# Kernel optimization log

Measured on AMD Instinct MI355X. Metric: run time of the kernel, lower is better.

The kernel has to match this reference:

```python
import jax, jax.numpy as jnp
import numpy as np

N = 50000       # nodes
E = 800000      # edges (before self-loops)
F_IN = 256      # input feature dim
HID = 32        # hidden per head
HEADS = 4
CLASSES = 32


def setup_inputs() -> dict:
    key = jax.random.key(0)
    ks = jax.random.split(key, 10)
    x = jax.random.normal(ks[0], (N, F_IN), dtype=jnp.float32)
    edge_index = jax.random.randint(ks[1], (2, E), 0, N, dtype=jnp.int32)
    s1 = 1.0 / np.sqrt(F_IN)
    s2 = 1.0 / np.sqrt(HEADS * HID)
    W1 = jax.random.normal(ks[2], (HEADS * HID, F_IN), dtype=jnp.float32) * s1
    a_src1 = jax.random.normal(ks[3], (HEADS, HID), dtype=jnp.float32) * 0.1
    a_dst1 = jax.random.normal(ks[4], (HEADS, HID), dtype=jnp.float32) * 0.1
    b1 = jnp.zeros((HEADS * HID,), dtype=jnp.float32)
    W2 = jax.random.normal(ks[5], (CLASSES, HEADS * HID), dtype=jnp.float32) * s2
    a_src2 = jax.random.normal(ks[6], (1, CLASSES), dtype=jnp.float32) * 0.1
    a_dst2 = jax.random.normal(ks[7], (1, CLASSES), dtype=jnp.float32) * 0.1
    b2 = jnp.zeros((CLASSES,), dtype=jnp.float32)
    return {"x": x, "edge_index": edge_index,
            "W1": W1, "a_src1": a_src1, "a_dst1": a_dst1, "b1": b1,
            "W2": W2, "a_src2": a_src2, "a_dst2": a_dst2, "b2": b2}


def gat_conv(x, src, dst, W, a_src, a_dst, b, heads, ch):
    """PyG GATConv: linear -> per-head additive attention -> segment softmax over dst -> scatter-sum."""
    n = x.shape[0]
    h = (x @ W.T).reshape(n, heads, ch)                      # [N,H,C]
    asc = jnp.einsum('nhc,hc->nh', h, a_src)                 # att_src . h_j
    adc = jnp.einsum('nhc,hc->nh', h, a_dst)                 # att_dst . h_i
    e = jax.nn.leaky_relu(asc[src] + adc[dst], 0.2)          # [E,H]
    m = jax.ops.segment_max(e, dst, num_segments=n)          # stable softmax per destination
    p = jnp.exp(e - m[dst])
    denom = jax.ops.segment_sum(p, dst, num_segments=n)
    alpha = p / (denom[dst] + 1e-16)                         # [E,H]
    out = jax.ops.segment_sum(h[src] * alpha[:, :, None], dst, num_segments=n)  # [N,H,C]
    return out.reshape(n, heads * ch) + b


def reference(x, edge_index, W1, a_src1, a_dst1, b1, W2, a_src2, a_dst2, b2):
    # PyG GATConv default add_self_loops=True
    loops = jnp.arange(N, dtype=edge_index.dtype)
    src = jnp.concatenate([edge_index[0], loops])
    dst = jnp.concatenate([edge_index[1], loops])
    h = gat_conv(x, src, dst, W1, a_src1, a_dst1, b1, HEADS, HID)
    h = jax.nn.relu(h)                                       # dropout is identity in eval mode
    out = gat_conv(h, src, dst, W2, a_src2, a_dst2, b2, 1, CLASSES)
    return jax.nn.log_softmax(out, axis=1)
```

## Files before the change

kernel.cpp:

```cpp
#include <hip/hip_runtime.h>
#include <hip/hip_fp16.h>

#define N_NODES 50000
#define E_EDGES 800000
#define ET (E_EDGES + N_NODES)
#define NBKT 1024
#define BCAP 2048
#define G1_BLOCKS 391
#define P_BLOCKS 250
#define P_EPB 3200

typedef _Float16 h8 __attribute__((ext_vector_type(8)));
typedef float f32x16 __attribute__((ext_vector_type(16)));

__device__ __forceinline__ float lrelu(float v) { return v > 0.f ? v : 0.2f * v; }

__global__ __launch_bounds__(256) void prep_kernel(const float* __restrict__ W1,
                                                   const float* __restrict__ W2,
                                                   const float* __restrict__ as1,
                                                   const float* __restrict__ ad1,
                                                   _Float16* __restrict__ w1h,
                                                   _Float16* __restrict__ w2h,
                                                   int* __restrict__ cursor) {
    int i = blockIdx.x * 256 + threadIdx.x;
    if (i < 1024) cursor[i] = 0;
    if (i < 4096) {
        int j = i * 8;
#pragma unroll
        for (int t = 0; t < 8; t++) w1h[j + t] = (_Float16)W1[j + t];
    } else if (i < 4608) {
        int j = (i - 4096) * 8;
#pragma unroll
        for (int t = 0; t < 8; t++) w2h[j + t] = (_Float16)W2[j + t];
    } else if (i < 5376) {
        int j = (i - 4608) * 8;
#pragma unroll
        for (int t = 0; t < 8; t++) w1h[136 * 256 + j + t] = (_Float16)0.f;
    } else if (i < 7424) {
        int a = i - 5376;
        int h = a >> 8, k = a & 255;
        const float* av = (h < 4 ? as1 : ad1) + (h & 3) * 32;
        const float* wb = W1 + (size_t)(h & 3) * 32 * 256 + k;
        float s = 0.f;
#pragma unroll
        for (int c = 0; c < 32; c++) s += av[c] * wb[(size_t)c * 256];
        w1h[(size_t)(128 + h) * 256 + k] = (_Float16)s;
    }
}

__global__ __launch_bounds__(256) void gp_kernel(const float* __restrict__ x,
                                                 const int* __restrict__ ei,
                                                 const _Float16* __restrict__ w1h,
                                                 _Float16* __restrict__ h1h,
                                                 float* __restrict__ asc1,
                                                 float* __restrict__ adc1,
                                                 int* __restrict__ cursor,
                                                 int* __restrict__ scratch) {
    __shared__ int hcnt[NBKT];
    __shared__ int hbase[NBKT];
    int tid = threadIdx.x;
    if (blockIdx.x >= G1_BLOCKS) {
        int b = blockIdx.x - G1_BLOCKS;
#pragma unroll
        for (int u = 0; u < NBKT / 256; u++) hcnt[u * 256 + tid] = 0;
        __syncthreads();
        int e0 = b * P_EPB;
        const int4* s4 = (const int4*)(ei + e0);
        const int4* d4 = (const int4*)(ei + E_EDGES + e0);
        for (int q = tid; q < P_EPB / 4; q += 256) {
            int4 d = d4[q];
            atomicAdd(&hcnt[d.x >> 6], 1);
            atomicAdd(&hcnt[d.y >> 6], 1);
            atomicAdd(&hcnt[d.z >> 6], 1);
            atomicAdd(&hcnt[d.w >> 6], 1);
        }
        __syncthreads();
#pragma unroll
        for (int u = 0; u < NBKT / 256; u++) {
            int bb = u * 256 + tid;
            int c = hcnt[bb];
            hbase[bb] = (c > 0) ? atomicAdd(&cursor[bb], c) : 0;
            hcnt[bb] = 0;
        }
        __syncthreads();
        for (int q = tid; q < P_EPB / 4; q += 256) {
            int4 s = s4[q];
            int4 d = d4[q];
            int bk, pos;
            bk = d.x >> 6; pos = hbase[bk] + atomicAdd(&hcnt[bk], 1);
            scratch[(size_t)bk * BCAP + pos] = s.x | ((d.x & 63) << 16);
            bk = d.y >> 6; pos = hbase[bk] + atomicAdd(&hcnt[bk], 1);
            scratch[(size_t)bk * BCAP + pos] = s.y | ((d.y & 63) << 16);
            bk = d.z >> 6; pos = hbase[bk] + atomicAdd(&hcnt[bk], 1);
            scratch[(size_t)bk * BCAP + pos] = s.z | ((d.z & 63) << 16);
            bk = d.w >> 6; pos = hbase[bk] + atomicAdd(&hcnt[bk], 1);
            scratch[(size_t)bk * BCAP + pos] = s.w | ((d.w & 63) << 16);
        }
        return;
    }
    int wid = tid >> 6, lane = tid & 63;
    int rbase = blockIdx.x * 128 + wid * 32;
    if (rbase >= N_NODES) return;
    int l31 = lane & 31, l5 = lane >> 5;
    int ar = rbase + l31;
    if (ar > N_NODES - 1) ar = N_NODES - 1;
    const float* ap = x + (size_t)ar * 256 + l5 * 8;
    const _Float16* bp = w1h + (size_t)l31 * 256 + l5 * 8;
    f32x16 acc0 = {}, acc1 = {}, acc2 = {}, acc3 = {}, acc4 = {};
#pragma unroll 4
    for (int ks = 0; ks < 16; ks++) {
        float4 xa = *(const float4*)(ap + ks * 16);
        float4 xb = *(const float4*)(ap + ks * 16 + 4);
        h8 av;
        av[0] = (_Float16)xa.x; av[1] = (_Float16)xa.y;
        av[2] = (_Float16)xa.z; av[3] = (_Float16)xa.w;
        av[4] = (_Float16)xb.x; av[5] = (_Float16)xb.y;
        av[6] = (_Float16)xb.z; av[7] = (_Float16)xb.w;
        h8 b0 = *(const h8*)(bp + ks * 16);
        h8 b1 = *(const h8*)(bp + 32 * 256 + ks * 16);
        h8 b2 = *(const h8*)(bp + 64 * 256 + ks * 16);
        h8 b3 = *(const h8*)(bp + 96 * 256 + ks * 16);
        h8 b4 = *(const h8*)(bp + 128 * 256 + ks * 16);
        acc0 = __builtin_amdgcn_mfma_f32_32x32x16_f16(av, b0, acc0, 0, 0, 0);
        acc1 = __builtin_amdgcn_mfma_f32_32x32x16_f16(av, b1, acc1, 0, 0, 0);
        acc2 = __builtin_amdgcn_mfma_f32_32x32x16_f16(av, b2, acc2, 0, 0, 0);
        acc3 = __builtin_amdgcn_mfma_f32_32x32x16_f16(av, b3, acc3, 0, 0, 0);
        acc4 = __builtin_amdgcn_mfma_f32_32x32x16_f16(av, b4, acc4, 0, 0, 0);
    }
#pragma unroll
    for (int j = 0; j < 16; j++) {
        int row = rbase + (j & 3) + 8 * (j >> 2) + 4 * l5;
        if (row < N_NODES) {
            h1h[(size_t)row * 128 + 0  + l31] = (_Float16)acc0[j];
            h1h[(size_t)row * 128 + 32 + l31] = (_Float16)acc1[j];
            h1h[(size_t)row * 128 + 64 + l31] = (_Float16)acc2[j];
            h1h[(size_t)row * 128 + 96 + l31] = (_Float16)acc3[j];
            float v4 = acc4[j];
            if (l31 < 4) asc1[(size_t)row * 4 + l31] = v4;
            else if (l31 < 8) adc1[(size_t)row * 4 + (l31 - 4)] = v4;
        }
    }
}

__global__ __launch_bounds__(256) void fine_kernel(const int* __restrict__ scratch,
                                                   const int* __restrict__ cursor,
                                                   const float* __restrict__ asc1,
                                                   const float* __restrict__ adc1,
                                                   int* __restrict__ off,
                                                   int4* __restrict__ combo,
                                                   int* __restrict__ srcs) {
    __shared__ int rec[BCAP];
    __shared__ int fh[64];
    __shared__ int fcur[64];
    __shared__ int red[256];
    int b = blockIdx.x;
    int tid = threadIdx.x;
    int cnt = cursor[b];
    int part = 0;
    for (int i = tid; i < b; i += 256) part += cursor[i];
    red[tid] = part;
    if (tid < 64) fh[tid] = (b * 64 + tid < N_NODES) ? 1 : 0;
    __syncthreads();
    for (int s = 128; s >= 1; s >>= 1) {
        if (tid < s) red[tid] += red[tid + s];
        __syncthreads();
    }
    int gbase = red[0] + b * 64;
    for (int k = tid; k < cnt; k += 256) {
        int r = scratch[(size_t)b * BCAP + k];
        rec[k] = r;
        atomicAdd(&fh[r >> 16], 1);
    }
    __syncthreads();
    if (tid < 64) {
        int v = fh[tid];
        int incl = v;
#pragma unroll
        for (int d = 1; d < 64; d <<= 1) {
            int u = __shfl_up(incl, d);
            if (tid >= d) incl += u;
        }
        int excl = incl - v;
        fcur[tid] = excl;
        int n = b * 64 + tid;
        if (n < N_NODES) off[n] = gbase + excl;
    }
    if (b == 781 && tid == 0) off[N_NODES] = ET;
    __syncthreads();
    if (tid < 64) {
        int n = b * 64 + tid;
        if (n < N_NODES) {
            int pos = gbase + atomicAdd(&fcur[tid], 1);
            float4 av = *(const float4*)(asc1 + (size_t)n * 4);
            float4 dv = *(const float4*)(adc1 + (size_t)n * 4);
            __half2 p01 = __floats2half2_rn(__expf(lrelu(av.x + dv.x)), __expf(lrelu(av.y + dv.y)));
            __half2 p23 = __floats2half2_rn(__expf(lrelu(av.z + dv.z)), __expf(lrelu(av.w + dv.w)));
            int4 o;
            o.x = n;
            o.y = *(int*)&p01;
            o.z = *(int*)&p23;
            o.w = 0;
            combo[pos] = o;
            srcs[pos] = n;
        }
    }
    for (int k = tid; k < cnt; k += 256) {
        int r = rec[k];
        int src = r & 0xFFFF;
        int fbin = r >> 16;
        int dst = b * 64 + fbin;
        int pos = gbase + atomicAdd(&fcur[fbin], 1);
        float4 av = *(const float4*)(asc1 + (size_t)src * 4);
        float4 dv = *(const float4*)(adc1 + (size_t)dst * 4);
        __half2 p01 = __floats2half2_rn(__expf(lrelu(av.x + dv.x)), __expf(lrelu(av.y + dv.y)));
        __half2 p23 = __floats2half2_rn(__expf(lrelu(av.z + dv.z)), __expf(lrelu(av.w + dv.w)));
        int4 o;
        o.x = src;
        o.y = *(int*)&p01;
        o.z = *(int*)&p23;
        o.w = 0;
        combo[pos] = o;
        srcs[pos] = src;
    }
}

__global__ __launch_bounds__(256) void agg1_kernel(const __half* __restrict__ h1h,
                                                   const int4* __restrict__ combo,
                                                   const float* __restrict__ b1,
                                                   const int* __restrict__ off,
                                                   __half* __restrict__ h1b) {
    int wid = threadIdx.x >> 6, lane = threadIdx.x & 63;
    int node = blockIdx.x * 4 + wid;
    if (node >= N_NODES) return;
    int hh = lane >> 4;
    const __half2* h1h2 = (const __half2*)h1h;
    int s0 = off[node], s1 = off[node + 1];
    float den = 0.f, a0 = 0.f, a1 = 0.f;
    int j = s0;
    for (; j + 8 <= s1; j += 8) {
        int4 c[8];
#pragma unroll
        for (int u = 0; u < 8; u++) c[u] = combo[j + u];
        __half2 hv[8];
#pragma unroll
        for (int u = 0; u < 8; u++) hv[u] = h1h2[(size_t)c[u].x * 64 + lane];
#pragma unroll
        for (int u = 0; u < 8; u++) {
            union { int u32; __half2 h; } v;
            v.u32 = (hh & 2) ? c[u].z : c[u].y;
            float p = __half2float((hh & 1) ? v.h.y : v.h.x);
            float2 f = __half22float2(hv[u]);
            den += p;
            a0 += p * f.x;
            a1 += p * f.y;
        }
    }
    for (; j + 4 <= s1; j += 4) {
        int4 c[4];
#pragma unroll
        for (int u = 0; u < 4; u++) c[u] = combo[j + u];
        __half2 hv[4];
#pragma unroll
        for (int u = 0; u < 4; u++) hv[u] = h1h2[(size_t)c[u].x * 64 + lane];
#pragma unroll
        for (int u = 0; u < 4; u++) {
            union { int u32; __half2 h; } v;
            v.u32 = (hh & 2) ? c[u].z : c[u].y;
            float p = __half2float((hh & 1) ? v.h.y : v.h.x);
            float2 f = __half22float2(hv[u]);
            den += p;
            a0 += p * f.x;
            a1 += p * f.y;
        }
    }
    for (; j < s1; j++) {
        int4 c = combo[j];
        union { int u32; __half2 h; } v;
        v.u32 = (hh & 2) ? c.z : c.y;
        float p = __half2float((hh & 1) ? v.h.y : v.h.x);
        float2 f = __half22float2(h1h2[(size_t)c.x * 64 + lane]);
        den += p;
        a0 += p * f.x;
        a1 += p * f.y;
    }
    float inv = 1.f / (den + 1e-16f);
    float o0 = fmaxf(a0 * inv + b1[2 * lane], 0.f);
    float o1 = fmaxf(a1 * inv + b1[2 * lane + 1], 0.f);
    ((__half2*)h1b)[(size_t)node * 64 + lane] = __floats2half2_rn(o0, o1);
}

__global__ __launch_bounds__(256) void gemm2_mfma(const __half* __restrict__ h1b,
                                                  const _Float16* __restrict__ w2h,
                                                  const float* __restrict__ as2,
                                                  const float* __restrict__ ad2,
                                                  __half* __restrict__ h2h,
                                                  float* __restrict__ asc2,
                                                  float* __restrict__ adc2) {
    int wid = threadIdx.x >> 6, lane = threadIdx.x & 63;
    int rbase = blockIdx.x * 128 + wid * 32;
    if (rbase >= N_NODES) return;
    int l31 = lane & 31, l5 = lane >> 5;
    int ar = rbase + l31;
    if (ar > N_NODES - 1) ar = N_NODES - 1;
    const _Float16* ap = (const _Float16*)h1b + (size_t)ar * 128 + l5 * 8;
    const _Float16* bp = w2h + (size_t)l31 * 128 + l5 * 8;
    f32x16 acc = {};
#pragma unroll
    for (int ks = 0; ks < 8; ks++) {
        h8 av = *(const h8*)(ap + ks * 16);
        h8 bv = *(const h8*)(bp + ks * 16);
        acc = __builtin_amdgcn_mfma_f32_32x32x16_f16(av, bv, acc, 0, 0, 0);
    }
    float asw = as2[l31], adw = ad2[l31];
#pragma unroll
    for (int j = 0; j < 16; j++) {
        int row = rbase + (j & 3) + 8 * (j >> 2) + 4 * l5;
        float v = acc[j];
        float sv = v * asw, dv = v * adw;
#pragma unroll
        for (int m = 1; m <= 16; m <<= 1) {
            sv += __shfl_xor(sv, m);
            dv += __shfl_xor(dv, m);
        }
        if (row < N_NODES) {
            h2h[(size_t)row * 32 + l31] = __float2half(v);
            if (l31 == 0) { asc2[row] = sv; adc2[row] = dv; }
        }
    }
}

__global__ __launch_bounds__(256) void agg2_kernel(const __half* __restrict__ h2h,
                                                   const int* __restrict__ srcs,
                                                   const float* __restrict__ asc2,
                                                   const float* __restrict__ adc2,
                                                   const float* __restrict__ b2,
                                                   const int* __restrict__ off,
                                                   float* __restrict__ out) {
    int wid = threadIdx.x >> 6, lane = threadIdx.x & 63;
    int node = blockIdx.x * 4 + wid;
    if (node >= N_NODES) return;
    int g = lane >> 4;
    int li = lane & 15;
    const __half2* h2h2 = (const __half2*)h2h;
    float adv = adc2[node];
    int s0 = off[node], s1 = off[node + 1];
    float den = 0.f, a0 = 0.f, a1 = 0.f;
    int j = s0 + g;
    for (; j + 16 <= s1; j += 16) {
        int s[4];
#pragma unroll
        for (int u = 0; u < 4; u++) s[u] = srcs[j + 4 * u];
        float av[4];
#pragma unroll
        for (int u = 0; u < 4; u++) av[u] = asc2[s[u]];
        __half2 hv[4];
#pragma unroll
        for (int u = 0; u < 4; u++) hv[u] = h2h2[(size_t)s[u] * 16 + li];
#pragma unroll
        for (int u = 0; u < 4; u++) {
            float p = __expf(lrelu(av[u] + adv));
            float2 f = __half22float2(hv[u]);
            den += p;
            a0 += p * f.x;
            a1 += p * f.y;
        }
    }
    for (; j < s1; j += 4) {
        int s = srcs[j];
        float p = __expf(lrelu(asc2[s] + adv));
        float2 f = __half22float2(h2h2[(size_t)s * 16 + li]);
        den += p;
        a0 += p * f.x;
        a1 += p * f.y;
    }
    den += __shfl_xor(den, 16); den += __shfl_xor(den, 32);
    a0 += __shfl_xor(a0, 16);  a0 += __shfl_xor(a0, 32);
    a1 += __shfl_xor(a1, 16);  a1 += __shfl_xor(a1, 32);
    float inv = 1.f / (den + 1e-16f);
    float v0 = a0 * inv + b2[2 * li];
    float v1 = a1 * inv + b2[2 * li + 1];
    float mx = fmaxf(v0, v1);
#pragma unroll
    for (int msk = 8; msk >= 1; msk >>= 1) mx = fmaxf(mx, __shfl_xor(mx, msk));
    float se = __expf(v0 - mx) + __expf(v1 - mx);
#pragma unroll
    for (int msk = 8; msk >= 1; msk >>= 1) se += __shfl_xor(se, msk);
    float lse = mx + __logf(se);
    if (lane < 16) {
        ((float2*)out)[(size_t)node * 16 + li] = make_float2(v0 - lse, v1 - lse);
    }
}

extern "C" void kernel_launch(void* const* d_in, const int* in_sizes, int n_in,
                              void* d_out, int out_size, void* d_ws, size_t ws_size,
                              hipStream_t stream) {
    const float* x   = (const float*)d_in[0];
    const int* ei    = (const int*)d_in[1];
    const float* W1  = (const float*)d_in[2];
    const float* as1 = (const float*)d_in[3];
    const float* ad1 = (const float*)d_in[4];
    const float* b1  = (const float*)d_in[5];
    const float* W2  = (const float*)d_in[6];
    const float* as2 = (const float*)d_in[7];
    const float* ad2 = (const float*)d_in[8];
    const float* b2  = (const float*)d_in[9];
    float* out = (float*)d_out;

    char* base = (char*)d_ws;
    int4* combo   = (int4*)base;
    int* scratch  = (int*)(base + 13600000);
    _Float16* w1h = (_Float16*)(base + 30377216);
    _Float16* w2h = (_Float16*)(base + 30459136);
    _Float16* h1h = (_Float16*)(base + 30467328);
    __half* h1b   = (__half*)(base + 43267328);
    __half* h2h   = (__half*)(base + 56067328);
    float* asc1   = (float*)(base + 59267328);
    float* adc1   = (float*)(base + 60067328);
    float* asc2   = (float*)(base + 60867328);
    float* adc2   = (float*)(base + 61067328);
    int* off      = (int*)(base + 61267328);
    int* cursor   = (int*)(base + 61467332);
    int* srcs     = (int*)(base + 61471428);

    prep_kernel<<<29, 256, 0, stream>>>(W1, W2, as1, ad1, w1h, w2h, cursor);
    gp_kernel<<<G1_BLOCKS + P_BLOCKS, 256, 0, stream>>>(x, ei, w1h, h1h, asc1, adc1, cursor, scratch);
    fine_kernel<<<782, 256, 0, stream>>>(scratch, cursor, asc1, adc1, off, combo, srcs);
    agg1_kernel<<<(N_NODES + 3) / 4, 256, 0, stream>>>((const __half*)h1h, combo, b1, off, h1b);
    gemm2_mfma<<<391, 256, 0, stream>>>(h1b, w2h, as2, ad2, h2h, asc2, adc2);
    agg2_kernel<<<(N_NODES + 3) / 4, 256, 0, stream>>>(h2h, srcs, asc2, adc2, b2, off, out);
}
```

Baseline: 138.9 us.

## Fuse fine CSR bucketing with layer-1 aggregation using shared-memory edge lists

Merges fine_kernel and agg1_kernel into a single 512-thread kernel. Each block builds its 64-destination edge list (sources and fp16 attention weights) in LDS and then aggregates those nodes directly from shared memory. This drops the global combo buffer write/read round trip and one kernel launch. In exchange, each block uses much more LDS, which can lower occupancy, and aggregation parallelism drops to 8 nodes per wave, serialised, in only 782 blocks. Degree imbalance within a bucket could also leave waves idle.

```diff
diff --git a/kernel.cpp b/kernel.cpp
--- a/kernel.cpp
+++ b/kernel.cpp
@@ -6,6 +6,7 @@
 #define ET (E_EDGES + N_NODES)
 #define NBKT 1024
 #define BCAP 2048
+#define SCAP 2112
 #define G1_BLOCKS 391
 #define P_BLOCKS 250
 #define P_EPB 3200
@@ -142,38 +143,45 @@
     }
 }
 
-__global__ __launch_bounds__(256) void fine_kernel(const int* __restrict__ scratch,
-                                                   const int* __restrict__ cursor,
-                                                   const float* __restrict__ asc1,
-                                                   const float* __restrict__ adc1,
-                                                   int* __restrict__ off,
-                                                   int4* __restrict__ combo,
-                                                   int* __restrict__ srcs) {
+__global__ __launch_bounds__(512) void fa_kernel(const int* __restrict__ scratch,
+                                                 const int* __restrict__ cursor,
+                                                 const float* __restrict__ asc1,
+                                                 const float* __restrict__ adc1,
+                                                 const __half* __restrict__ h1h,
+                                                 const float* __restrict__ b1,
+                                                 int* __restrict__ off,
+                                                 int* __restrict__ srcs,
+                                                 __half* __restrict__ h1b) {
     __shared__ int rec[BCAP];
+    __shared__ int ssrc[SCAP];
+    __shared__ int sp01[SCAP];
+    __shared__ int sp23[SCAP];
     __shared__ int fh[64];
     __shared__ int fcur[64];
-    __shared__ int red[256];
+    __shared__ int lstart[64];
+    __shared__ int red[512];
     int b = blockIdx.x;
     int tid = threadIdx.x;
     int cnt = cursor[b];
     int part = 0;
-    for (int i = tid; i < b; i += 256) part += cursor[i];
+    for (int i = tid; i < b; i += 512) part += cursor[i];
     red[tid] = part;
-    if (tid < 64) fh[tid] = (b * 64 + tid < N_NODES) ? 1 : 0;
+    if (tid < 64) fh[tid] = 0;
     __syncthreads();
-    for (int s = 128; s >= 1; s >>= 1) {
+    for (int s = 256; s >= 1; s >>= 1) {
         if (tid < s) red[tid] += red[tid + s];
         __syncthreads();
     }
     int gbase = red[0] + b * 64;
-    for (int k = tid; k < cnt; k += 256) {
+    for (int k = tid; k < cnt; k += 512) {
         int r = scratch[(size_t)b * BCAP + k];
         rec[k] = r;
         atomicAdd(&fh[r >> 16], 1);
     }
     __syncthreads();
     if (tid < 64) {
-        int v = fh[tid];
+        int n = b * 64 + tid;
+        int v = fh[tid] + ((n < N_NODES) ? 1 : 0);
         int incl = v;
 #pragma unroll
         for (int d = 1; d < 64; d <<= 1) {
@@ -181,8 +189,8 @@
             if (tid >= d) incl += u;
         }
         int excl = incl - v;
-        fcur[tid] = excl;
-        int n = b * 64 + tid;
+        lstart[tid] = excl;
+        fcur[tid] = excl + ((n < N_NODES) ? 1 : 0);
         if (n < N_NODES) off[n] = gbase + excl;
     }
     if (b == 781 && tid == 0) off[N_NODES] = ET;
@@ -190,103 +198,102 @@
     if (tid < 64) {
         int n = b * 64 + tid;
         if (n < N_NODES) {
-            int pos = gbase + atomicAdd(&fcur[tid], 1);
+            int pos = lstart[tid];
             float4 av = *(const float4*)(asc1 + (size_t)n * 4);
             float4 dv = *(const float4*)(adc1 + (size_t)n * 4);
             __half2 p01 = __floats2half2_rn(__expf(lrelu(av.x + dv.x)), __expf(lrelu(av.y + dv.y)));
             __half2 p23 = __floats2half2_rn(__expf(lrelu(av.z + dv.z)), __expf(lrelu(av.w + dv.w)));
-            int4 o;
-            o.x = n;
-            o.y = *(int*)&p01;
-            o.z = *(int*)&p23;
-            o.w = 0;
-            combo[pos] = o;
-            srcs[pos] = n;
-        }
-    }
-    for (int k = tid; k < cnt; k += 256) {
+            ssrc[pos] = n;
+            sp01[pos] = *(int*)&p01;
+            sp23[pos] = *(int*)&p23;
+            srcs[gbase + pos] = n;
+        }
+    }
+    for (int k = tid; k < cnt; k += 512) {
         int r = rec[k];
         int src = r & 0xFFFF;
         int fbin = r >> 16;
         int dst = b * 64 + fbin;
-        int pos = gbase + atomicAdd(&fcur[fbin], 1);
+        int pos = atomicAdd(&fcur[fbin], 1);
         float4 av = *(const float4*)(asc1 + (size_t)src * 4);
         float4 dv = *(const float4*)(adc1 + (size_t)dst * 4);
         __half2 p01 = __floats2half2_rn(__expf(lrelu(av.x + dv.x)), __expf(lrelu(av.y + dv.y)));
         __half2 p23 = __floats2half2_rn(__expf(lrelu(av.z + dv.z)), __expf(lrelu(av.w + dv.w)));
-        int4 o;
-        o.x = src;
-        o.y = *(int*)&p01;
-        o.z = *(int*)&p23;
-        o.w = 0;
-        combo[pos] = o;
-        srcs[pos] = src;
-    }
-}
-
-__global__ __launch_bounds__(256) void agg1_kernel(const __half* __restrict__ h1h,
-                                                   const int4* __restrict__ combo,
-                                                   const float* __restrict__ b1,
-                                                   const int* __restrict__ off,
-                                                   __half* __restrict__ h1b) {
-    int wid = threadIdx.x >> 6, lane = threadIdx.x & 63;
-    int node = blockIdx.x * 4 + wid;
-    if (node >= N_NODES) return;
+        ssrc[pos] = src;
+        sp01[pos] = *(int*)&p01;
+        sp23[pos] = *(int*)&p23;
+        srcs[gbase + pos] = src;
+    }
+    __syncthreads();
+    int wid = tid >> 6, lane = tid & 63;
     int hh = lane >> 4;
     const __half2* h1h2 = (const __half2*)h1h;
-    int s0 = off[node], s1 = off[node + 1];
-    float den = 0.f, a0 = 0.f, a1 = 0.f;
-    int j = s0;
-    for (; j + 8 <= s1; j += 8) {
-        int4 c[8];
-#pragma unroll
-        for (int u = 0; u < 8; u++) c[u] = combo[j + u];
-        __half2 hv[8];
-#pragma unroll
-        for (int u = 0; u < 8; u++) hv[u] = h1h2[(size_t)c[u].x * 64 + lane];
-#pragma unroll
-        for (int u = 0; u < 8; u++) {
+    float bl0 = b1[2 * lane], bl1 = b1[2 * lane + 1];
+    for (int ln = wid * 8; ln < wid * 8 + 8; ln++) {
+        int node = b * 64 + ln;
+        if (node >= N_NODES) break;
+        int s0l = lstart[ln];
+        int s1l = fcur[ln];
+        float den = 0.f, a0 = 0.f, a1 = 0.f;
+        int j = s0l;
+        for (; j + 8 <= s1l; j += 8) {
+            int src8[8];
+            int pv[8];
+#pragma unroll
+            for (int u = 0; u < 8; u++) {
+                src8[u] = ssrc[j + u];
+                pv[u] = (hh & 2) ? sp23[j + u] : sp01[j + u];
+            }
+            __half2 hv[8];
+#pragma unroll
+            for (int u = 0; u < 8; u++) hv[u] = h1h2[(size_t)src8[u] * 64 + lane];
+#pragma unroll
+            for (int u = 0; u < 8; u++) {
+                union { int u32; __half2 h; } v;
+                v.u32 = pv[u];
+                float p = __half2float((hh & 1) ? v.h.y : v.h.x);
+                float2 f = __half22float2(hv[u]);
+                den += p;
+                a0 += p * f.x;
+                a1 += p * f.y;
+            }
+        }
+        for (; j + 4 <= s1l; j += 4) {
+            int src4[4];
+            int pv[4];
+#pragma unroll
+            for (int u = 0; u < 4; u++) {
+                src4[u] = ssrc[j + u];
+                pv[u] = (hh & 2) ? sp23[j + u] : sp01[j + u];
+            }
+            __half2 hv[4];
+#pragma unroll
+            for (int u = 0; u < 4; u++) hv[u] = h1h2[(size_t)src4[u] * 64 + lane];
+#pragma unroll
+            for (int u = 0; u < 4; u++) {
+                union { int u32; __half2 h; } v;
+                v.u32 = pv[u];
+                float p = __half2float((hh & 1) ? v.h.y : v.h.x);
+                float2 f = __half22float2(hv[u]);
+                den += p;
+                a0 += p * f.x;
+                a1 += p * f.y;
+            }
+        }
+        for (; j < s1l; j++) {
             union { int u32; __half2 h; } v;
-            v.u32 = (hh & 2) ? c[u].z : c[u].y;
+            v.u32 = (hh & 2) ? sp23[j] : sp01[j];
             float p = __half2float((hh & 1) ? v.h.y : v.h.x);
-            float2 f = __half22float2(hv[u]);
+            float2 f = __half22float2(h1h2[(size_t)ssrc[j] * 64 + lane]);
             den += p;
             a0 += p * f.x;
             a1 += p * f.y;
         }
-    }
-    for (; j + 4 <= s1; j += 4) {
-        int4 c[4];
-#pragma unroll
-        for (int u = 0; u < 4; u++) c[u] = combo[j + u];
-        __half2 hv[4];
-#pragma unroll
-        for (int u = 0; u < 4; u++) hv[u] = h1h2[(size_t)c[u].x * 64 + lane];
-#pragma unroll
-        for (int u = 0; u < 4; u++) {
-            union { int u32; __half2 h; } v;
-            v.u32 = (hh & 2) ? c[u].z : c[u].y;
-            float p = __half2float((hh & 1) ? v.h.y : v.h.x);
-            float2 f = __half22float2(hv[u]);
-            den += p;
-            a0 += p * f.x;
-            a1 += p * f.y;
-        }
-    }
-    for (; j < s1; j++) {
-        int4 c = combo[j];
-        union { int u32; __half2 h; } v;
-        v.u32 = (hh & 2) ? c.z : c.y;
-        float p = __half2float((hh & 1) ? v.h.y : v.h.x);
-        float2 f = __half22float2(h1h2[(size_t)c.x * 64 + lane]);
-        den += p;
-        a0 += p * f.x;
-        a1 += p * f.y;
-    }
-    float inv = 1.f / (den + 1e-16f);
-    float o0 = fmaxf(a0 * inv + b1[2 * lane], 0.f);
-    float o1 = fmaxf(a1 * inv + b1[2 * lane + 1], 0.f);
-    ((__half2*)h1b)[(size_t)node * 64 + lane] = __floats2half2_rn(o0, o1);
+        float inv = 1.f / (den + 1e-16f);
+        float o0 = fmaxf(a0 * inv + bl0, 0.f);
+        float o1 = fmaxf(a1 * inv + bl1, 0.f);
+        ((__half2*)h1b)[(size_t)node * 64 + lane] = __floats2half2_rn(o0, o1);
+    }
 }
 
 __global__ __launch_bounds__(256) void gemm2_mfma(const __half* __restrict__ h1b,
@@ -407,7 +414,6 @@
     float* out = (float*)d_out;
 
     char* base = (char*)d_ws;
-    int4* combo   = (int4*)base;
     int* scratch  = (int*)(base + 13600000);
     _Float16* w1h = (_Float16*)(base + 30377216);
     _Float16* w2h = (_Float16*)(base + 30459136);
@@ -424,8 +430,7 @@
 
     prep_kernel<<<29, 256, 0, stream>>>(W1, W2, as1, ad1, w1h, w2h, cursor);
     gp_kernel<<<G1_BLOCKS + P_BLOCKS, 256, 0, stream>>>(x, ei, w1h, h1h, asc1, adc1, cursor, scratch);
-    fine_kernel<<<782, 256, 0, stream>>>(scratch, cursor, asc1, adc1, off, combo, srcs);
-    agg1_kernel<<<(N_NODES + 3) / 4, 256, 0, stream>>>((const __half*)h1h, combo, b1, off, h1b);
+    fa_kernel<<<782, 512, 0, stream>>>(scratch, cursor, asc1, adc1, (const __half*)h1h, b1, off, srcs, h1b);
     gemm2_mfma<<<391, 256, 0, stream>>>(h1b, w2h, as2, ad2, h2h, asc2, adc2);
     agg2_kernel<<<(N_NODES + 3) / 4, 256, 0, stream>>>(h2h, srcs, asc2, adc2, b2, off, out);
 }
```

New measurement: 122.6 us. 1.13x faster.
